# Kernel tuning notes

Measured on AMD Instinct MI355X. Metric: run time of the kernel, lower is better.

Reference implementation:

```python
import jax, jax.numpy as jnp
import numpy as np


def setup_inputs() -> dict:
    key = jax.random.key(0)
    ks = jax.random.split(key, 7)
    B, T, E, H = 256, 512, 256, 256
    s = 1.0 / np.sqrt(E + H)
    return {
        "embedding": jax.random.normal(ks[0], (B, T, E), dtype=jnp.float32),
        "Wz": jax.random.normal(ks[1], (H, E + H), dtype=jnp.float32) * s,
        "bz": jax.random.normal(ks[2], (H,), dtype=jnp.float32) * s,
        "Wr": jax.random.normal(ks[3], (H, E + H), dtype=jnp.float32) * s,
        "br": jax.random.normal(ks[4], (H,), dtype=jnp.float32) * s,
        "Wm": jax.random.normal(ks[5], (H, E + H), dtype=jnp.float32) * s,
        "bm": jax.random.normal(ks[6], (H,), dtype=jnp.float32) * s,
    }


def reference(embedding, Wz, bz, Wr, br, Wm, bm):
    # embedding: [B, T, E] -> time-major [T, B, E] (matches Encoder.forward transpose)
    emb = jnp.transpose(embedding, (1, 0, 2))
    B = emb.shape[1]
    H = Wz.shape[0]
    h0 = jnp.zeros((B, H), dtype=embedding.dtype)

    def step(h, x):  # x: [B, E], h: [B, H]
        xi = jnp.concatenate([x, h], axis=1)            # [B, E+H]
        z = jax.nn.sigmoid(xi @ Wz.T + bz)              # update gate
        r = jax.nn.sigmoid(xi @ Wr.T + br)              # reset gate
        xm = jnp.concatenate([x, r * h], axis=1)
        h_cand = jnp.tanh(xm @ Wm.T + bm)
        h_new = (1.0 - z) * h + z * h_cand
        return h_new, h_new

    _, hs = jax.lax.scan(step, h0, emb)                 # hs: [T, B, H]
    return jnp.transpose(hs, (1, 0, 2))                 # [B, T, H]
```

## Files before the change

### kernel.cpp

```cpp
#include <hip/hip_runtime.h>

typedef _Float16 half8_t __attribute__((ext_vector_type(8)));
typedef _Float16 half2_t __attribute__((ext_vector_type(2)));
typedef float floatx4 __attribute__((ext_vector_type(4)));

#define B_DIM 256
#define T_DIM 512
#define E_DIM 256
#define H_DIM 256
#define MROWS (B_DIM * T_DIM)

__device__ __forceinline__ half2_t mk2(_Float16 x, _Float16 y) {
    half2_t v; v[0] = x; v[1] = y; return v;
}

__device__ __forceinline__ void dma1k(const void* g, void* l, int lane) {
    __builtin_amdgcn_global_load_lds(
        (const __attribute__((address_space(1))) unsigned int*)
            ((const char*)g + lane * 16),
        (__attribute__((address_space(3))) unsigned int*)l,
        16, 0, 0);
}

__global__ __launch_bounds__(256, 2) void gemm_x(
    const float* __restrict__ emb,
    const float* __restrict__ Wz, const float* __restrict__ bz,
    const float* __restrict__ Wr, const float* __restrict__ br,
    const float* __restrict__ Wm, const float* __restrict__ bm,
    _Float16* __restrict__ Xz, _Float16* __restrict__ Xr,
    float* __restrict__ Xm)
{
    const int n0 = blockIdx.x * 128;
    const int m0 = blockIdx.y * 128;
    const int gate = n0 >> 8;
    const int ng0 = n0 & 255;
    const float* W    = (gate == 0) ? Wz : (gate == 1) ? Wr : Wm;
    const float* bias = (gate == 0) ? bz : (gate == 1) ? br : bm;

    __shared__ __align__(16) _Float16 lA[128 * 40];
    __shared__ __align__(16) _Float16 lB[128 * 40];

    const int t = threadIdx.x;
    const int lane = t & 63;
    const int wave = t >> 6;
    const int wm = (wave >> 1) * 64;
    const int wn = (wave & 1) * 64;
    const int lq = lane >> 4;
    const int lr = lane & 15;

    floatx4 acc[4][4];
    #pragma unroll
    for (int i = 0; i < 4; ++i)
        #pragma unroll
        for (int j = 0; j < 4; ++j)
            acc[i][j] = (floatx4)0.0f;

    const int srow = t >> 1;
    const int scol = (t & 1) * 16;
    const float* aSrc = emb + (size_t)(m0 + srow) * E_DIM + scol;
    const float* bSrc = W + (size_t)(ng0 + srow) * (E_DIM + H_DIM) + scol;

    for (int k0 = 0; k0 < E_DIM; k0 += 32) {
        float ta[16], tb[16];
        #pragma unroll
        for (int u = 0; u < 4; ++u) {
            *(float4*)(ta + 4 * u) = *(const float4*)(aSrc + k0 + 4 * u);
            *(float4*)(tb + 4 * u) = *(const float4*)(bSrc + k0 + 4 * u);
        }
        half8_t a0, a1, b0, b1;
        #pragma unroll
        for (int u = 0; u < 8; ++u) {
            a0[u] = (_Float16)ta[u]; a1[u] = (_Float16)ta[u + 8];
            b0[u] = (_Float16)tb[u]; b1[u] = (_Float16)tb[u + 8];
        }
        __syncthreads();
        *(half8_t*)&lA[srow * 40 + scol]     = a0;
        *(half8_t*)&lA[srow * 40 + scol + 8] = a1;
        *(half8_t*)&lB[srow * 40 + scol]     = b0;
        *(half8_t*)&lB[srow * 40 + scol + 8] = b1;
        __syncthreads();

        half8_t af[4], bf[4];
        #pragma unroll
        for (int i = 0; i < 4; ++i)
            af[i] = *(const half8_t*)&lA[(wm + i * 16 + lr) * 40 + lq * 8];
        #pragma unroll
        for (int j = 0; j < 4; ++j)
            bf[j] = *(const half8_t*)&lB[(wn + j * 16 + lr) * 40 + lq * 8];
        #pragma unroll
        for (int i = 0; i < 4; ++i)
            #pragma unroll
            for (int j = 0; j < 4; ++j)
                acc[i][j] = __builtin_amdgcn_mfma_f32_16x16x32_f16(
                    af[i], bf[j], acc[i][j], 0, 0, 0);
    }

    if (gate < 2) {
        _Float16* dst = (gate == 0) ? Xz : Xr;
        #pragma unroll
        for (int j = 0; j < 4; ++j) {
            const int ng = ng0 + wn + j * 16 + lr;
            const float bv = bias[ng];
            #pragma unroll
            for (int i = 0; i < 4; ++i) {
                const int mrow = m0 + wm + i * 16 + lq * 4;
                #pragma unroll
                for (int r = 0; r < 4; ++r)
                    dst[(size_t)(mrow + r) * H_DIM + ng] =
                        (_Float16)(acc[i][j][r] + bv);
            }
        }
    } else {
        #pragma unroll
        for (int j = 0; j < 4; ++j) {
            const int ng = ng0 + wn + j * 16 + lr;
            const float bv = bias[ng];
            #pragma unroll
            for (int i = 0; i < 4; ++i) {
                const int mrow = m0 + wm + i * 16 + lq * 4;
                #pragma unroll
                for (int r = 0; r < 4; ++r)
                    Xm[(size_t)(mrow + r) * H_DIM + ng] = acc[i][j][r] + bv;
            }
        }
    }
}

__device__ __forceinline__ float pick4(floatx4 v, int r) {
    float x01 = (r & 1) ? v[1] : v[0];
    float x23 = (r & 1) ? v[3] : v[2];
    return (r & 2) ? x23 : x01;
}

__global__ __launch_bounds__(512, 2) void gru_rec(
    const float* __restrict__ Wz,
    const float* __restrict__ Wr,
    const float* __restrict__ Wm,
    const _Float16* __restrict__ Xz,
    const _Float16* __restrict__ Xr,
    float* __restrict__ out)
{
    const int b = blockIdx.x;
    const int t = threadIdx.x;
    const int w    = t >> 6;
    const int lane = t & 63;
    const int lr   = lane & 15;
    const int lq   = lane >> 4;

    __shared__ __align__(16) _Float16 hh[256];
    __shared__ __align__(16) float    hf[256];
    __shared__ __align__(16) _Float16 rh[256];
    __shared__ __align__(16) float    zl[256];
    __shared__ __align__(16) _Float16 xzS[4096];
    __shared__ __align__(16) _Float16 xrS[4096];
    __shared__ __align__(16) float    xmS[4096];
    __shared__ __align__(16) float    hist[2048];

    half8_t af[4][8];
    {
        const float* Wg = (w < 4) ? Wz : Wr;
        #pragma unroll
        for (int i = 0; i < 4; ++i) {
            const float* rp = Wg +
                (size_t)(((w & 3) * 4 + i) * 16 + lr) * (E_DIM + H_DIM) +
                E_DIM + lq * 8;
            #pragma unroll
            for (int kt = 0; kt < 8; ++kt) {
                float4 f0 = *(const float4*)(rp + kt * 32);
                float4 f1 = *(const float4*)(rp + kt * 32 + 4);
                half8_t hv;
                hv[0] = (_Float16)f0.x; hv[1] = (_Float16)f0.y;
                hv[2] = (_Float16)f0.z; hv[3] = (_Float16)f0.w;
                hv[4] = (_Float16)f1.x; hv[5] = (_Float16)f1.y;
                hv[6] = (_Float16)f1.z; hv[7] = (_Float16)f1.w;
                af[i][kt] = hv;
            }
        }
    }
    half8_t am[2][8];
    {
        #pragma unroll
        for (int i = 0; i < 2; ++i) {
            const float* rp = Wm +
                (size_t)((w * 2 + i) * 16 + lr) * (E_DIM + H_DIM) +
                E_DIM + lq * 8;
            #pragma unroll
            for (int kt = 0; kt < 8; ++kt) {
                float4 f0 = *(const float4*)(rp + kt * 32);
                float4 f1 = *(const float4*)(rp + kt * 32 + 4);
                half8_t hv;
                hv[0] = (_Float16)f0.x; hv[1] = (_Float16)f0.y;
                hv[2] = (_Float16)f0.z; hv[3] = (_Float16)f0.w;
                hv[4] = (_Float16)f1.x; hv[5] = (_Float16)f1.y;
                hv[6] = (_Float16)f1.z; hv[7] = (_Float16)f1.w;
                am[i][kt] = hv;
            }
        }
    }

    const int rowA = (w & 3) * 64 + (lr >> 2) * 16 + lq * 4 + (lr & 3);
    const int row2 = w * 32 + ((lr >> 2) & 1) * 16 + lq * 4 + (lr & 3);

    const size_t rowbase = (size_t)b * T_DIM * H_DIM;
    const _Float16* XgS = (w < 4) ? xzS : xrS;

    auto stage_block = [&](int row0, int buf) {
        const size_t base = rowbase + (size_t)row0 * H_DIM;
        #pragma unroll
        for (int qq = 0; qq < 2; ++qq) {
            const int q = w * 2 + qq;
            if (q < 4)
                dma1k(Xz + base + q * 512,
                      (void*)(xzS + buf * 2048 + q * 512), lane);
            else if (q < 8)
                dma1k(Xr + base + (q - 4) * 512,
                      (void*)(xrS + buf * 2048 + (q - 4) * 512), lane);
            else
                dma1k(out + base + (q - 8) * 256,
                      (void*)(xmS + buf * 2048 + (q - 8) * 256), lane);
        }
    };

    stage_block(0, 0);
    if (t < 256) { hh[t] = (_Float16)0.0f; hf[t] = 0.0f; }
    __syncthreads();

    for (int ts8 = 0; ts8 < T_DIM; ts8 += 8) {
        const int cur = (ts8 >> 3) & 1;
        #pragma unroll
        for (int j = 0; j < 8; ++j) {
            if (j == 7 && ts8 + 8 < T_DIM)
                stage_block(ts8 + 8, cur ^ 1);

            floatx4 acc[4];
            acc[0] = (floatx4)0.0f; acc[1] = (floatx4)0.0f;
            acc[2] = (floatx4)0.0f; acc[3] = (floatx4)0.0f;
            #pragma unroll
            for (int kt = 0; kt < 8; ++kt) {
                half8_t bf = *(const half8_t*)&hh[kt * 32 + lq * 8];
                #pragma unroll
                for (int i = 0; i < 4; ++i)
                    acc[i] = __builtin_amdgcn_mfma_f32_16x16x32_f16(
                        af[i][kt], bf, acc[i], 0, 0, 0);
            }
            {
                const int r = lr & 3;
                float s0 = pick4(acc[0], r), s1 = pick4(acc[1], r);
                float s2 = pick4(acc[2], r), s3 = pick4(acc[3], r);
                float v = (lr & 8) ? ((lr & 4) ? s3 : s2)
                                   : ((lr & 4) ? s1 : s0);
                const float a = v + (float)XgS[cur * 2048 + j * 256 + rowA];
                const float g = 1.0f / (1.0f + __expf(-a));
                if (w < 4) zl[rowA] = g;
                else       rh[rowA] = (_Float16)(g * hf[rowA]);
            }
            __syncthreads();

            floatx4 acc2[2];
            acc2[0] = (floatx4)0.0f; acc2[1] = (floatx4)0.0f;
            #pragma unroll
            for (int kt = 0; kt < 8; ++kt) {
                half8_t bfm = *(const half8_t*)&rh[kt * 32 + lq * 8];
                #pragma unroll
                for (int i = 0; i < 2; ++i)
                    acc2[i] = __builtin_amdgcn_mfma_f32_16x16x32_f16(
                        am[i][kt], bfm, acc2[i], 0, 0, 0);
            }
            if (lr < 8) {
                const int r = lr & 3;
                float u0 = pick4(acc2[0], r), u1 = pick4(acc2[1], r);
                float v2 = (lr & 4) ? u1 : u0;
                const float amv = v2 + xmS[cur * 2048 + j * 256 + row2];
                const float hc  = 2.0f / (1.0f + __expf(-2.0f * amv)) - 1.0f;
                const float z   = zl[row2];
                const float hp  = hf[row2];
                const float hn  = hp + z * (hc - hp);
                hist[j * 256 + row2] = hn;
                hf[row2] = hn;
                hh[row2] = (_Float16)hn;
            }
            __syncthreads();
        }

        {
            const float4 hv4 = *(const float4*)&hist[t * 4];
            *(float4*)&out[rowbase + (size_t)ts8 * H_DIM + t * 4] = hv4;
        }
    }
}

extern "C" void kernel_launch(void* const* d_in, const int* in_sizes, int n_in,
                              void* d_out, int out_size, void* d_ws, size_t ws_size,
                              hipStream_t stream) {
    (void)in_sizes; (void)n_in; (void)out_size; (void)ws_size;
    const float* emb = (const float*)d_in[0];
    const float* Wz  = (const float*)d_in[1];
    const float* bz  = (const float*)d_in[2];
    const float* Wr  = (const float*)d_in[3];
    const float* br  = (const float*)d_in[4];
    const float* Wm  = (const float*)d_in[5];
    const float* bm  = (const float*)d_in[6];
    float* out = (float*)d_out;

    _Float16* Xz = (_Float16*)d_ws;
    _Float16* Xr = Xz + (size_t)MROWS * H_DIM;

    dim3 g1(6, MROWS / 128);
    gemm_x<<<g1, 256, 0, stream>>>(emb, Wz, bz, Wr, br, Wm, bm, Xz, Xr, out);
    gru_rec<<<B_DIM, 512, 0, stream>>>(Wz, Wr, Wm, Xz, Xr, out);
}
```

Baseline: 1.048 ms.

## Split GRU recurrence across 16 waves and loop gate tiles in projection GEMM

The recurrent kernel now runs 1024 threads per batch row instead of 512. Each wave holds half as many Wz/Wr and Wm register fragments and issues fewer MFMAs per step, which shortens the serial per-timestep critical path. The input-projection GEMM now launches one block per 128-row M tile and loops over all six gate N tiles inside the block, reloading the embedding tile each time. This trades launch parallelism for fewer blocks and reuse of the A rows through cache. It also brings more barrier participants per step and lower occupancy in the GEMM.

```diff
diff --git a/kernel.cpp b/kernel.cpp
--- a/kernel.cpp
+++ b/kernel.cpp
@@ -1,7 +1,6 @@
 #include <hip/hip_runtime.h>
 
 typedef _Float16 half8_t __attribute__((ext_vector_type(8)));
-typedef _Float16 half2_t __attribute__((ext_vector_type(2)));
 typedef float floatx4 __attribute__((ext_vector_type(4)));
 
 #define B_DIM 256
@@ -9,10 +8,6 @@
 #define E_DIM 256
 #define H_DIM 256
 #define MROWS (B_DIM * T_DIM)
-
-__device__ __forceinline__ half2_t mk2(_Float16 x, _Float16 y) {
-    half2_t v; v[0] = x; v[1] = y; return v;
-}
 
 __device__ __forceinline__ void dma1k(const void* g, void* l, int lane) {
     __builtin_amdgcn_global_load_lds(
@@ -30,12 +25,7 @@
     _Float16* __restrict__ Xz, _Float16* __restrict__ Xr,
     float* __restrict__ Xm)
 {
-    const int n0 = blockIdx.x * 128;
-    const int m0 = blockIdx.y * 128;
-    const int gate = n0 >> 8;
-    const int ng0 = n0 & 255;
-    const float* W    = (gate == 0) ? Wz : (gate == 1) ? Wr : Wm;
-    const float* bias = (gate == 0) ? bz : (gate == 1) ? br : bm;
+    const int m0 = blockIdx.x * 128;
 
     __shared__ __align__(16) _Float16 lA[128 * 40];
     __shared__ __align__(16) _Float16 lB[128 * 40];
@@ -48,79 +38,86 @@
     const int lq = lane >> 4;
     const int lr = lane & 15;
 
-    floatx4 acc[4][4];
-    #pragma unroll
-    for (int i = 0; i < 4; ++i)
-        #pragma unroll
-        for (int j = 0; j < 4; ++j)
-            acc[i][j] = (floatx4)0.0f;
-
     const int srow = t >> 1;
     const int scol = (t & 1) * 16;
     const float* aSrc = emb + (size_t)(m0 + srow) * E_DIM + scol;
-    const float* bSrc = W + (size_t)(ng0 + srow) * (E_DIM + H_DIM) + scol;
-
-    for (int k0 = 0; k0 < E_DIM; k0 += 32) {
-        float ta[16], tb[16];
-        #pragma unroll
-        for (int u = 0; u < 4; ++u) {
-            *(float4*)(ta + 4 * u) = *(const float4*)(aSrc + k0 + 4 * u);
-            *(float4*)(tb + 4 * u) = *(const float4*)(bSrc + k0 + 4 * u);
-        }
-        half8_t a0, a1, b0, b1;
-        #pragma unroll
-        for (int u = 0; u < 8; ++u) {
-            a0[u] = (_Float16)ta[u]; a1[u] = (_Float16)ta[u + 8];
-            b0[u] = (_Float16)tb[u]; b1[u] = (_Float16)tb[u + 8];
-        }
-        __syncthreads();
-        *(half8_t*)&lA[srow * 40 + scol]     = a0;
-        *(half8_t*)&lA[srow * 40 + scol + 8] = a1;
-        *(half8_t*)&lB[srow * 40 + scol]     = b0;
-        *(half8_t*)&lB[srow * 40 + scol + 8] = b1;
-        __syncthreads();
-
-        half8_t af[4], bf[4];
+
+    for (int nt = 0; nt < 6; ++nt) {
+        const int gate = nt >> 1;
+        const int ng0 = (nt & 1) * 128;
+        const float* W    = (gate == 0) ? Wz : (gate == 1) ? Wr : Wm;
+        const float* bias = (gate == 0) ? bz : (gate == 1) ? br : bm;
+        const float* bSrc = W + (size_t)(ng0 + srow) * (E_DIM + H_DIM) + scol;
+
+        floatx4 acc[4][4];
         #pragma unroll
         for (int i = 0; i < 4; ++i)
-            af[i] = *(const half8_t*)&lA[(wm + i * 16 + lr) * 40 + lq * 8];
-        #pragma unroll
-        for (int j = 0; j < 4; ++j)
-            bf[j] = *(const half8_t*)&lB[(wn + j * 16 + lr) * 40 + lq * 8];
-        #pragma unroll
-        for (int i = 0; i < 4; ++i)
             #pragma unroll
             for (int j = 0; j < 4; ++j)
-                acc[i][j] = __builtin_amdgcn_mfma_f32_16x16x32_f16(
-                    af[i], bf[j], acc[i][j], 0, 0, 0);
-    }
-
-    if (gate < 2) {
-        _Float16* dst = (gate == 0) ? Xz : Xr;
-        #pragma unroll
-        for (int j = 0; j < 4; ++j) {
-            const int ng = ng0 + wn + j * 16 + lr;
-            const float bv = bias[ng];
-            #pragma unroll
-            for (int i = 0; i < 4; ++i) {
-                const int mrow = m0 + wm + i * 16 + lq * 4;
+                acc[i][j] = (floatx4)0.0f;
+
+        for (int k0 = 0; k0 < E_DIM; k0 += 32) {
+            float ta[16], tb[16];
+            #pragma unroll
+            for (int u = 0; u < 4; ++u) {
+                *(float4*)(ta + 4 * u) = *(const float4*)(aSrc + k0 + 4 * u);
+                *(float4*)(tb + 4 * u) = *(const float4*)(bSrc + k0 + 4 * u);
+            }
+            half8_t a0, a1, b0, b1;
+            #pragma unroll
+            for (int u = 0; u < 8; ++u) {
+                a0[u] = (_Float16)ta[u]; a1[u] = (_Float16)ta[u + 8];
+                b0[u] = (_Float16)tb[u]; b1[u] = (_Float16)tb[u + 8];
+            }
+            __syncthreads();
+            *(half8_t*)&lA[srow * 40 + scol]     = a0;
+            *(half8_t*)&lA[srow * 40 + scol + 8] = a1;
+            *(half8_t*)&lB[srow * 40 + scol]     = b0;
+            *(half8_t*)&lB[srow * 40 + scol + 8] = b1;
+            __syncthreads();
+
+            half8_t af[4], bf[4];
+            #pragma unroll
+            for (int i = 0; i < 4; ++i)
+                af[i] = *(const half8_t*)&lA[(wm + i * 16 + lr) * 40 + lq * 8];
+            #pragma unroll
+            for (int j = 0; j < 4; ++j)
+                bf[j] = *(const half8_t*)&lB[(wn + j * 16 + lr) * 40 + lq * 8];
+            #pragma unroll
+            for (int i = 0; i < 4; ++i)
                 #pragma unroll
-                for (int r = 0; r < 4; ++r)
-                    dst[(size_t)(mrow + r) * H_DIM + ng] =
-                        (_Float16)(acc[i][j][r] + bv);
-            }
-        }
-    } else {
-        #pragma unroll
-        for (int j = 0; j < 4; ++j) {
-            const int ng = ng0 + wn + j * 16 + lr;
-            const float bv = bias[ng];
-            #pragma unroll
-            for (int i = 0; i < 4; ++i) {
-                const int mrow = m0 + wm + i * 16 + lq * 4;
+                for (int j = 0; j < 4; ++j)
+                    acc[i][j] = __builtin_amdgcn_mfma_f32_16x16x32_f16(
+                        af[i], bf[j], acc[i][j], 0, 0, 0);
+        }
+
+        if (gate < 2) {
+            _Float16* dst = (gate == 0) ? Xz : Xr;
+            #pragma unroll
+            for (int j = 0; j < 4; ++j) {
+                const int ng = ng0 + wn + j * 16 + lr;
+                const float bv = bias[ng];
                 #pragma unroll
-                for (int r = 0; r < 4; ++r)
-                    Xm[(size_t)(mrow + r) * H_DIM + ng] = acc[i][j][r] + bv;
+                for (int i = 0; i < 4; ++i) {
+                    const int mrow = m0 + wm + i * 16 + lq * 4;
+                    #pragma unroll
+                    for (int r = 0; r < 4; ++r)
+                        dst[(size_t)(mrow + r) * H_DIM + ng] =
+                            (_Float16)(acc[i][j][r] + bv);
+                }
+            }
+        } else {
+            #pragma unroll
+            for (int j = 0; j < 4; ++j) {
+                const int ng = ng0 + wn + j * 16 + lr;
+                const float bv = bias[ng];
+                #pragma unroll
+                for (int i = 0; i < 4; ++i) {
+                    const int mrow = m0 + wm + i * 16 + lq * 4;
+                    #pragma unroll
+                    for (int r = 0; r < 4; ++r)
+                        Xm[(size_t)(mrow + r) * H_DIM + ng] = acc[i][j][r] + bv;
+                }
             }
         }
     }
@@ -132,7 +129,7 @@
     return (r & 2) ? x23 : x01;
 }
 
-__global__ __launch_bounds__(512, 2) void gru_rec(
+__global__ __launch_bounds__(1024, 1) void gru_rec(
     const float* __restrict__ Wz,
     const float* __restrict__ Wr,
     const float* __restrict__ Wm,
@@ -156,13 +153,13 @@
     __shared__ __align__(16) float    xmS[4096];
     __shared__ __align__(16) float    hist[2048];
 
-    half8_t af[4][8];
+    half8_t af[2][8];
     {
-        const float* Wg = (w < 4) ? Wz : Wr;
-        #pragma unroll
-        for (int i = 0; i < 4; ++i) {
+        const float* Wg = (w < 8) ? Wz : Wr;
+        #pragma unroll
+        for (int i = 0; i < 2; ++i) {
             const float* rp = Wg +
-                (size_t)(((w & 3) * 4 + i) * 16 + lr) * (E_DIM + H_DIM) +
+                (size_t)(((w & 7) * 2 + i) * 16 + lr) * (E_DIM + H_DIM) +
                 E_DIM + lq * 8;
             #pragma unroll
             for (int kt = 0; kt < 8; ++kt) {
@@ -177,48 +174,41 @@
             }
         }
     }
-    half8_t am[2][8];
+    half8_t am[8];
     {
-        #pragma unroll
-        for (int i = 0; i < 2; ++i) {
-            const float* rp = Wm +
-                (size_t)((w * 2 + i) * 16 + lr) * (E_DIM + H_DIM) +
-                E_DIM + lq * 8;
-            #pragma unroll
-            for (int kt = 0; kt < 8; ++kt) {
-                float4 f0 = *(const float4*)(rp + kt * 32);
-                float4 f1 = *(const float4*)(rp + kt * 32 + 4);
-                half8_t hv;
-                hv[0] = (_Float16)f0.x; hv[1] = (_Float16)f0.y;
-                hv[2] = (_Float16)f0.z; hv[3] = (_Float16)f0.w;
-                hv[4] = (_Float16)f1.x; hv[5] = (_Float16)f1.y;
-                hv[6] = (_Float16)f1.z; hv[7] = (_Float16)f1.w;
-                am[i][kt] = hv;
-            }
-        }
-    }
-
-    const int rowA = (w & 3) * 64 + (lr >> 2) * 16 + lq * 4 + (lr & 3);
-    const int row2 = w * 32 + ((lr >> 2) & 1) * 16 + lq * 4 + (lr & 3);
+        const float* rp = Wm +
+            (size_t)(w * 16 + lr) * (E_DIM + H_DIM) + E_DIM + lq * 8;
+        #pragma unroll
+        for (int kt = 0; kt < 8; ++kt) {
+            float4 f0 = *(const float4*)(rp + kt * 32);
+            float4 f1 = *(const float4*)(rp + kt * 32 + 4);
+            half8_t hv;
+            hv[0] = (_Float16)f0.x; hv[1] = (_Float16)f0.y;
+            hv[2] = (_Float16)f0.z; hv[3] = (_Float16)f0.w;
+            hv[4] = (_Float16)f1.x; hv[5] = (_Float16)f1.y;
+            hv[6] = (_Float16)f1.z; hv[7] = (_Float16)f1.w;
+            am[kt] = hv;
+        }
+    }
+
+    const int rowA = (w & 7) * 32 + ((lr >> 2) & 1) * 16 + lq * 4 + (lr & 3);
+    const int rowB = w * 16 + lq * 4 + (lr & 3);
 
     const size_t rowbase = (size_t)b * T_DIM * H_DIM;
-    const _Float16* XgS = (w < 4) ? xzS : xrS;
+    const _Float16* XgS = (w < 8) ? xzS : xrS;
 
     auto stage_block = [&](int row0, int buf) {
         const size_t base = rowbase + (size_t)row0 * H_DIM;
-        #pragma unroll
-        for (int qq = 0; qq < 2; ++qq) {
-            const int q = w * 2 + qq;
-            if (q < 4)
-                dma1k(Xz + base + q * 512,
-                      (void*)(xzS + buf * 2048 + q * 512), lane);
-            else if (q < 8)
-                dma1k(Xr + base + (q - 4) * 512,
-                      (void*)(xrS + buf * 2048 + (q - 4) * 512), lane);
-            else
-                dma1k(out + base + (q - 8) * 256,
-                      (void*)(xmS + buf * 2048 + (q - 8) * 256), lane);
-        }
+        const int q = w;
+        if (q < 4)
+            dma1k(Xz + base + q * 512,
+                  (void*)(xzS + buf * 2048 + q * 512), lane);
+        else if (q < 8)
+            dma1k(Xr + base + (q - 4) * 512,
+                  (void*)(xrS + buf * 2048 + (q - 4) * 512), lane);
+        else
+            dma1k(out + base + (q - 8) * 256,
+                  (void*)(xmS + buf * 2048 + (q - 8) * 256), lane);
     };
 
     stage_block(0, 0);
@@ -232,59 +222,50 @@
             if (j == 7 && ts8 + 8 < T_DIM)
                 stage_block(ts8 + 8, cur ^ 1);
 
-            floatx4 acc[4];
-            acc[0] = (floatx4)0.0f; acc[1] = (floatx4)0.0f;
-            acc[2] = (floatx4)0.0f; acc[3] = (floatx4)0.0f;
+            floatx4 acc0 = (floatx4)0.0f, acc1 = (floatx4)0.0f;
             #pragma unroll
             for (int kt = 0; kt < 8; ++kt) {
                 half8_t bf = *(const half8_t*)&hh[kt * 32 + lq * 8];
-                #pragma unroll
-                for (int i = 0; i < 4; ++i)
-                    acc[i] = __builtin_amdgcn_mfma_f32_16x16x32_f16(
-                        af[i][kt], bf, acc[i], 0, 0, 0);
-            }
-            {
+                acc0 = __builtin_amdgcn_mfma_f32_16x16x32_f16(
+                    af[0][kt], bf, acc0, 0, 0, 0);
+                acc1 = __builtin_amdgcn_mfma_f32_16x16x32_f16(
+                    af[1][kt], bf, acc1, 0, 0, 0);
+            }
+            if (lr < 8) {
                 const int r = lr & 3;
-                float s0 = pick4(acc[0], r), s1 = pick4(acc[1], r);
-                float s2 = pick4(acc[2], r), s3 = pick4(acc[3], r);
-                float v = (lr & 8) ? ((lr & 4) ? s3 : s2)
-                                   : ((lr & 4) ? s1 : s0);
+                float s0 = pick4(acc0, r), s1 = pick4(acc1, r);
+                float v = (lr & 4) ? s1 : s0;
                 const float a = v + (float)XgS[cur * 2048 + j * 256 + rowA];
                 const float g = 1.0f / (1.0f + __expf(-a));
-                if (w < 4) zl[rowA] = g;
+                if (w < 8) zl[rowA] = g;
                 else       rh[rowA] = (_Float16)(g * hf[rowA]);
             }
             __syncthreads();
 
-            floatx4 acc2[2];
-            acc2[0] = (floatx4)0.0f; acc2[1] = (floatx4)0.0f;
+            floatx4 acc2 = (floatx4)0.0f;
             #pragma unroll
             for (int kt = 0; kt < 8; ++kt) {
                 half8_t bfm = *(const half8_t*)&rh[kt * 32 + lq * 8];
-                #pragma unroll
-                for (int i = 0; i < 2; ++i)
-                    acc2[i] = __builtin_amdgcn_mfma_f32_16x16x32_f16(
-                        am[i][kt], bfm, acc2[i], 0, 0, 0);
-            }
-            if (lr < 8) {
-                const int r = lr & 3;
-                float u0 = pick4(acc2[0], r), u1 = pick4(acc2[1], r);
-                float v2 = (lr & 4) ? u1 : u0;
-                const float amv = v2 + xmS[cur * 2048 + j * 256 + row2];
+                acc2 = __builtin_amdgcn_mfma_f32_16x16x32_f16(
+                    am[kt], bfm, acc2, 0, 0, 0);
+            }
+            if (lr < 4) {
+                const float v2  = pick4(acc2, lr & 3);
+                const float amv = v2 + xmS[cur * 2048 + j * 256 + rowB];
                 const float hc  = 2.0f / (1.0f + __expf(-2.0f * amv)) - 1.0f;
-                const float z   = zl[row2];
-                const float hp  = hf[row2];
+                const float z   = zl[rowB];
+                const float hp  = hf[rowB];
                 const float hn  = hp + z * (hc - hp);
-                hist[j * 256 + row2] = hn;
-                hf[row2] = hn;
-                hh[row2] = (_Float16)hn;
+                hist[j * 256 + rowB] = hn;
+                hf[rowB] = hn;
+                hh[rowB] = (_Float16)hn;
             }
             __syncthreads();
         }
 
         {
-            const float4 hv4 = *(const float4*)&hist[t * 4];
-            *(float4*)&out[rowbase + (size_t)ts8 * H_DIM + t * 4] = hv4;
+            const float2 hv2 = *(const float2*)&hist[t * 2];
+            *(float2*)&out[rowbase + (size_t)ts8 * H_DIM + t * 2] = hv2;
         }
     }
 }
@@ -305,7 +286,7 @@
     _Float16* Xz = (_Float16*)d_ws;
     _Float16* Xr = Xz + (size_t)MROWS * H_DIM;
 
-    dim3 g1(6, MROWS / 128);
+    dim3 g1(MROWS / 128);
     gemm_x<<<g1, 256, 0, stream>>>(emb, Wz, bz, Wr, br, Wm, bm, Xz, Xr, out);
-    gru_rec<<<B_DIM, 512, 0, stream>>>(Wz, Wr, Wm, Xz, Xr, out);
-}
+    gru_rec<<<B_DIM, 1024, 0, stream>>>(Wz, Wr, Wm, Xz, Xr, out);
+}
```

Result: slower. 1.119 ms (+6.9%).

## Keep full-K embedding tile resident in LDS and loop over all gate tiles

Applied to the files above, without the earlier changes.

The input-projection GEMM now launches one block per 128-row slab of the embedding. Each block converts that whole 128x256 slab to fp16 once into LDS and then iterates over all six 128-wide gate/column tiles, so the embedding is no longer re-read and re-converted six times. A small pre-kernel converts the gate weights to fp16 in workspace when space allows, and the LDS tiles use an XOR swizzle to avoid bank conflicts. The cost is large LDS use per block, which limits each CU to one block, and load and compute phases that are not overlapped.

```diff
diff --git a/kernel.cpp b/kernel.cpp
--- a/kernel.cpp
+++ b/kernel.cpp
@@ -1,7 +1,7 @@
 #include <hip/hip_runtime.h>
 
 typedef _Float16 half8_t __attribute__((ext_vector_type(8)));
-typedef _Float16 half2_t __attribute__((ext_vector_type(2)));
+typedef _Float16 half4_t __attribute__((ext_vector_type(4)));
 typedef float floatx4 __attribute__((ext_vector_type(4)));
 
 #define B_DIM 256
@@ -9,10 +9,6 @@
 #define E_DIM 256
 #define H_DIM 256
 #define MROWS (B_DIM * T_DIM)
-
-__device__ __forceinline__ half2_t mk2(_Float16 x, _Float16 y) {
-    half2_t v; v[0] = x; v[1] = y; return v;
-}
 
 __device__ __forceinline__ void dma1k(const void* g, void* l, int lane) {
     __builtin_amdgcn_global_load_lds(
@@ -22,23 +18,34 @@
         16, 0, 0);
 }
 
-__global__ __launch_bounds__(256, 2) void gemm_x(
+__global__ void cvt_w(const float* __restrict__ Wz,
+                      const float* __restrict__ Wr,
+                      const float* __restrict__ Wm,
+                      _Float16* __restrict__ Wf16)
+{
+    const int g = blockIdx.y;
+    const float* W = (g == 0) ? Wz : (g == 1) ? Wr : Wm;
+    const size_t i4 = ((size_t)blockIdx.x * 256 + threadIdx.x) * 4;
+    float4 f = *(const float4*)(W + i4);
+    half4_t h;
+    h[0] = (_Float16)f.x; h[1] = (_Float16)f.y;
+    h[2] = (_Float16)f.z; h[3] = (_Float16)f.w;
+    *(half4_t*)(Wf16 + (size_t)g * (256 * 512) + i4) = h;
+}
+
+__global__ __launch_bounds__(256, 1) void gemm_x(
     const float* __restrict__ emb,
     const float* __restrict__ Wz, const float* __restrict__ bz,
     const float* __restrict__ Wr, const float* __restrict__ br,
     const float* __restrict__ Wm, const float* __restrict__ bm,
+    const _Float16* __restrict__ Wf16,
     _Float16* __restrict__ Xz, _Float16* __restrict__ Xr,
     float* __restrict__ Xm)
 {
-    const int n0 = blockIdx.x * 128;
-    const int m0 = blockIdx.y * 128;
-    const int gate = n0 >> 8;
-    const int ng0 = n0 & 255;
-    const float* W    = (gate == 0) ? Wz : (gate == 1) ? Wr : Wm;
-    const float* bias = (gate == 0) ? bz : (gate == 1) ? br : bm;
-
-    __shared__ __align__(16) _Float16 lA[128 * 40];
-    __shared__ __align__(16) _Float16 lB[128 * 40];
+    const int m0 = blockIdx.x * 128;
+
+    __shared__ __align__(16) _Float16 lA[128 * 256];
+    __shared__ __align__(16) _Float16 lB[128 * 256];
 
     const int t = threadIdx.x;
     const int lane = t & 63;
@@ -48,81 +55,120 @@
     const int lq = lane >> 4;
     const int lr = lane & 15;
 
-    floatx4 acc[4][4];
-    #pragma unroll
-    for (int i = 0; i < 4; ++i)
-        #pragma unroll
-        for (int j = 0; j < 4; ++j)
-            acc[i][j] = (floatx4)0.0f;
-
-    const int srow = t >> 1;
-    const int scol = (t & 1) * 16;
-    const float* aSrc = emb + (size_t)(m0 + srow) * E_DIM + scol;
-    const float* bSrc = W + (size_t)(ng0 + srow) * (E_DIM + H_DIM) + scol;
-
-    for (int k0 = 0; k0 < E_DIM; k0 += 32) {
-        float ta[16], tb[16];
-        #pragma unroll
-        for (int u = 0; u < 4; ++u) {
-            *(float4*)(ta + 4 * u) = *(const float4*)(aSrc + k0 + 4 * u);
-            *(float4*)(tb + 4 * u) = *(const float4*)(bSrc + k0 + 4 * u);
-        }
-        half8_t a0, a1, b0, b1;
-        #pragma unroll
-        for (int u = 0; u < 8; ++u) {
-            a0[u] = (_Float16)ta[u]; a1[u] = (_Float16)ta[u + 8];
-            b0[u] = (_Float16)tb[u]; b1[u] = (_Float16)tb[u + 8];
+    {
+        const int row  = t >> 1;
+        const int colb = (t & 1) * 128;
+        const float* src = emb + (size_t)(m0 + row) * E_DIM + colb;
+        char* dst = (char*)lA + row * 512;
+        const int sw = (row & 7) << 4;
+        #pragma unroll
+        for (int c = 0; c < 16; ++c) {
+            float4 f0 = *(const float4*)(src + c * 8);
+            float4 f1 = *(const float4*)(src + c * 8 + 4);
+            half8_t hv;
+            hv[0] = (_Float16)f0.x; hv[1] = (_Float16)f0.y;
+            hv[2] = (_Float16)f0.z; hv[3] = (_Float16)f0.w;
+            hv[4] = (_Float16)f1.x; hv[5] = (_Float16)f1.y;
+            hv[6] = (_Float16)f1.z; hv[7] = (_Float16)f1.w;
+            *(half8_t*)(dst + (((colb + c * 8) * 2) ^ sw)) = hv;
+        }
+    }
+    __syncthreads();
+
+    const int swf = (lr & 7) << 4;
+
+    for (int nt = 0; nt < 6; ++nt) {
+        const int gate = nt >> 1;
+        const int ng0 = (nt & 1) * 128;
+        const float* bias = (gate == 0) ? bz : (gate == 1) ? br : bm;
+
+        {
+            const int row  = t >> 1;
+            const int colb = (t & 1) * 128;
+            char* dst = (char*)lB + row * 512;
+            const int sw = (row & 7) << 4;
+            if (Wf16) {
+                const _Float16* src = Wf16 + (size_t)gate * (256 * 512) +
+                                      (size_t)(ng0 + row) * 512 + colb;
+                #pragma unroll
+                for (int c = 0; c < 16; ++c)
+                    *(half8_t*)(dst + (((colb + c * 8) * 2) ^ sw)) =
+                        *(const half8_t*)(src + c * 8);
+            } else {
+                const float* W = (gate == 0) ? Wz : (gate == 1) ? Wr : Wm;
+                const float* src = W + (size_t)(ng0 + row) * 512 + colb;
+                #pragma unroll
+                for (int c = 0; c < 16; ++c) {
+                    float4 f0 = *(const float4*)(src + c * 8);
+                    float4 f1 = *(const float4*)(src + c * 8 + 4);
+                    half8_t hv;
+                    hv[0] = (_Float16)f0.x; hv[1] = (_Float16)f0.y;
+                    hv[2] = (_Float16)f0.z; hv[3] = (_Float16)f0.w;
+                    hv[4] = (_Float16)f1.x; hv[5] = (_Float16)f1.y;
+                    hv[6] = (_Float16)f1.z; hv[7] = (_Float16)f1.w;
+                    *(half8_t*)(dst + (((colb + c * 8) * 2) ^ sw)) = hv;
+                }
+            }
         }
         __syncthreads();
-        *(half8_t*)&lA[srow * 40 + scol]     = a0;
-        *(half8_t*)&lA[srow * 40 + scol + 8] = a1;
-        *(half8_t*)&lB[srow * 40 + scol]     = b0;
-        *(half8_t*)&lB[srow * 40 + scol + 8] = b1;
+
+        floatx4 acc[4][4];
+        #pragma unroll
+        for (int i = 0; i < 4; ++i)
+            #pragma unroll
+            for (int j = 0; j < 4; ++j)
+                acc[i][j] = (floatx4)0.0f;
+
+        #pragma unroll
+        for (int k0 = 0; k0 < 8; ++k0) {
+            const int kb = k0 * 64 + lq * 16;
+            half8_t af[4], bf[4];
+            #pragma unroll
+            for (int i = 0; i < 4; ++i)
+                af[i] = *(const half8_t*)
+                    ((const char*)lA + (wm + i * 16 + lr) * 512 + (kb ^ swf));
+            #pragma unroll
+            for (int j = 0; j < 4; ++j)
+                bf[j] = *(const half8_t*)
+                    ((const char*)lB + (wn + j * 16 + lr) * 512 + (kb ^ swf));
+            #pragma unroll
+            for (int i = 0; i < 4; ++i)
+                #pragma unroll
+                for (int j = 0; j < 4; ++j)
+                    acc[i][j] = __builtin_amdgcn_mfma_f32_16x16x32_f16(
+                        af[i], bf[j], acc[i][j], 0, 0, 0);
+        }
+
+        if (gate < 2) {
+            _Float16* dst = (gate == 0) ? Xz : Xr;
+            #pragma unroll
+            for (int j = 0; j < 4; ++j) {
+                const int ng = ng0 + wn + j * 16 + lr;
+                const float bv = bias[ng];
+                #pragma unroll
+                for (int i = 0; i < 4; ++i) {
+                    const int mrow = m0 + wm + i * 16 + lq * 4;
+                    #pragma unroll
+                    for (int r = 0; r < 4; ++r)
+                        dst[(size_t)(mrow + r) * H_DIM + ng] =
+                            (_Float16)(acc[i][j][r] + bv);
+                }
+            }
+        } else {
+            #pragma unroll
+            for (int j = 0; j < 4; ++j) {
+                const int ng = ng0 + wn + j * 16 + lr;
+                const float bv = bias[ng];
+                #pragma unroll
+                for (int i = 0; i < 4; ++i) {
+                    const int mrow = m0 + wm + i * 16 + lq * 4;
+                    #pragma unroll
+                    for (int r = 0; r < 4; ++r)
+                        Xm[(size_t)(mrow + r) * H_DIM + ng] = acc[i][j][r] + bv;
+                }
+            }
+        }
         __syncthreads();
-
-        half8_t af[4], bf[4];
-        #pragma unroll
-        for (int i = 0; i < 4; ++i)
-            af[i] = *(const half8_t*)&lA[(wm + i * 16 + lr) * 40 + lq * 8];
-        #pragma unroll
-        for (int j = 0; j < 4; ++j)
-            bf[j] = *(const half8_t*)&lB[(wn + j * 16 + lr) * 40 + lq * 8];
-        #pragma unroll
-        for (int i = 0; i < 4; ++i)
-            #pragma unroll
-            for (int j = 0; j < 4; ++j)
-                acc[i][j] = __builtin_amdgcn_mfma_f32_16x16x32_f16(
-                    af[i], bf[j], acc[i][j], 0, 0, 0);
-    }
-
-    if (gate < 2) {
-        _Float16* dst = (gate == 0) ? Xz : Xr;
-        #pragma unroll
-        for (int j = 0; j < 4; ++j) {
-            const int ng = ng0 + wn + j * 16 + lr;
-            const float bv = bias[ng];
-            #pragma unroll
-            for (int i = 0; i < 4; ++i) {
-                const int mrow = m0 + wm + i * 16 + lq * 4;
-                #pragma unroll
-                for (int r = 0; r < 4; ++r)
-                    dst[(size_t)(mrow + r) * H_DIM + ng] =
-                        (_Float16)(acc[i][j][r] + bv);
-            }
-        }
-    } else {
-        #pragma unroll
-        for (int j = 0; j < 4; ++j) {
-            const int ng = ng0 + wn + j * 16 + lr;
-            const float bv = bias[ng];
-            #pragma unroll
-            for (int i = 0; i < 4; ++i) {
-                const int mrow = m0 + wm + i * 16 + lq * 4;
-                #pragma unroll
-                for (int r = 0; r < 4; ++r)
-                    Xm[(size_t)(mrow + r) * H_DIM + ng] = acc[i][j][r] + bv;
-            }
-        }
     }
 }
 
@@ -292,7 +338,7 @@
 extern "C" void kernel_launch(void* const* d_in, const int* in_sizes, int n_in,
                               void* d_out, int out_size, void* d_ws, size_t ws_size,
                               hipStream_t stream) {
-    (void)in_sizes; (void)n_in; (void)out_size; (void)ws_size;
+    (void)in_sizes; (void)n_in; (void)out_size;
     const float* emb = (const float*)d_in[0];
     const float* Wz  = (const float*)d_in[1];
     const float* bz  = (const float*)d_in[2];
@@ -305,7 +351,14 @@
     _Float16* Xz = (_Float16*)d_ws;
     _Float16* Xr = Xz + (size_t)MROWS * H_DIM;
 
-    dim3 g1(6, MROWS / 128);
-    gemm_x<<<g1, 256, 0, stream>>>(emb, Wz, bz, Wr, br, Wm, bm, Xz, Xr, out);
+    const size_t xBytes = (size_t)MROWS * H_DIM * 2 * 2;
+    const size_t wBytes = (size_t)3 * 256 * 512 * 2;
+    _Float16* Wf16 = (ws_size >= xBytes + wBytes)
+                   ? (Xr + (size_t)MROWS * H_DIM) : (_Float16*)nullptr;
+
+    if (Wf16)
+        cvt_w<<<dim3(128, 3), 256, 0, stream>>>(Wz, Wr, Wm, Wf16);
+    gemm_x<<<dim3(MROWS / 128), 256, 0, stream>>>(
+        emb, Wz, bz, Wr, br, Wm, bm, Wf16, Xz, Xr, out);
     gru_rec<<<B_DIM, 512, 0, stream>>>(Wz, Wr, Wm, Xz, Xr, out);
 }
```

New measurement: 1.006 ms. -4.0%, faster.
